# Optimization experiments

Hardware: AMD Instinct MI355X
Metric: run time of the kernel (lower is better)

Reference implementation:

```python
import jax, jax.numpy as jnp
import numpy as np

N = 4096
FIN = 256
FOUT = 256
H = 1  # num_heads MUST be 1: edge projections reshape [N,N,H] -> (1,N,N)
NEG_MASK = -1000000.0
LRELU_SLOPE = 0.2
ESP = 1e-06
LN_EPS = 1e-05


def setup_inputs() -> dict:
    key = jax.random.key(0)
    ks = jax.random.split(key, 9)
    nodes_features = jax.random.normal(ks[0], (N, FIN), dtype=jnp.float32)
    degree_matrix = jax.random.normal(ks[1], (N, N), dtype=jnp.float32)
    edges_features_distance = jax.random.uniform(ks[2], (N, N), dtype=jnp.float32)
    edges_features_bond = jax.random.uniform(ks[3], (N, N), dtype=jnp.float32)
    # learned parameters (xavier-ish scale)
    proj_param = jax.random.normal(ks[4], (H, FIN, FOUT), dtype=jnp.float32) * (1.0 / np.sqrt(FIN))
    a_src = jax.random.normal(ks[5], (H, FOUT, 1), dtype=jnp.float32) * (1.0 / np.sqrt(FOUT))
    a_tgt = jax.random.normal(ks[6], (H, FOUT, 1), dtype=jnp.float32) * (1.0 / np.sqrt(FOUT))
    w_dist = jax.random.normal(ks[7], (H, 1), dtype=jnp.float32)  # nn.Linear(1, H).weight
    w_bond = jax.random.normal(ks[8], (H, 1), dtype=jnp.float32)
    return {
        "nodes_features": nodes_features,
        "degree_matrix": degree_matrix,
        "edges_features_distance": edges_features_distance,
        "edges_features_bond": edges_features_bond,
        "proj_param": proj_param,
        "a_src": a_src,
        "a_tgt": a_tgt,
        "w_dist": w_dist,
        "w_bond": w_bond,
        "cutoff": 0,
    }


def reference(nodes_features, degree_matrix, edges_features_distance,
              edges_features_bond, proj_param, a_src, a_tgt, w_dist, w_bond,
              cutoff=0):
    n = nodes_features.shape[0]
    h, fin, fout = proj_param.shape
    # connectivity mask: keep degree where positive, else large negative
    connectivity_mask = jnp.where(degree_matrix > 0, degree_matrix, NEG_MASK)
    # node projection: [H, N, Fout] (dropout is identity in eval)
    proj = jnp.einsum('nf,hfo->hno', nodes_features, proj_param)
    # attention scores: outer-sum of per-node source/target scores
    s_src = jnp.einsum('hno,hoi->hni', proj, a_src)      # [H, N, 1]
    s_tgt = jnp.einsum('hno,hoi->hni', proj, a_tgt)      # [H, N, 1]
    all_scores = jax.nn.leaky_relu(s_src + jnp.swapaxes(s_tgt, 1, 2), LRELU_SLOPE)  # [H,N,N]
    # edge contributions: Linear(1, H) on scalar edge features, reshaped (1,N,N) (H==1)
    dist_c = ((-edges_features_distance)[..., None] * w_dist[:, 0]).reshape(1, n, n)
    bond_c = (edges_features_bond[..., None] * w_bond[:, 0]).reshape(1, n, n)
    all_scores = all_scores + dist_c + bond_c
    # masked softmax over neighbors
    attn = jax.nn.softmax(all_scores + connectivity_mask[None], axis=-1)  # [H,N,N]
    # weighted aggregation
    out = jnp.einsum('hnm,hmo->hno', attn, proj)  # [H, N, Fout]
    # faithful to torch: transpose(2,1) -> [H,Fout,N] then contiguous view(-1,H,Fout)
    out = jnp.transpose(out, (0, 2, 1)).reshape(-1, h, fout)
    # concat heads (skip connection and bias are disabled per init args)
    out = out.reshape(-1, h * fout)
    out = jax.nn.elu(out)  # ELU activation, alpha=1
    # ---- no_grad connectivity update ----
    o = jax.lax.stop_gradient(out)
    dm = jax.lax.stop_gradient(degree_matrix)
    sim = o @ o.T                                        # [N, N]
    decay = -jax.lax.stop_gradient(edges_features_distance)
    upd = jax.nn.sigmoid(sim) * decay * (dm > 0).astype(o.dtype)
    upd = upd + ESP
    mean = jnp.mean(upd, axis=-1, keepdims=True)
    var = jnp.mean(jnp.square(upd - mean), axis=-1, keepdims=True)
    upd = (upd - mean) / jnp.sqrt(var + LN_EPS)          # layer_norm, no affine
    upd = upd + upd.T
    return out, upd
```

## Files before the change

kernel.cpp:

```cpp
#include <hip/hip_runtime.h>


using f32x4  = __attribute__((ext_vector_type(4))) float;
using bf16x8 = __attribute__((ext_vector_type(8))) __bf16;
using bf16x4 = __attribute__((ext_vector_type(4))) __bf16;
using u32x4  = __attribute__((ext_vector_type(4))) unsigned int;

__global__ __launch_bounds__(256) void prep_kernel(const float* __restrict__ x,
                                                   __bf16* __restrict__ y,
                                                   const float* __restrict__ w,
                                                   __bf16* __restrict__ wt,
                                                   float* __restrict__ Lrow,
                                                   float* __restrict__ ssrc,
                                                   float* __restrict__ stgt) {
  const int bx = blockIdx.x;
  if (bx < 1024) {
    int i = (bx * 256 + threadIdx.x) * 4;
    f32x4 v = *(const f32x4*)(x + i);
    bf16x4 o = { (__bf16)v[0], (__bf16)v[1], (__bf16)v[2], (__bf16)v[3] };
    *(bf16x4*)(y + i) = o;
  } else {
    int wb = bx - 1024;
    int i = wb * 256 + threadIdx.x;
    int o = i >> 8, f = i & 255;
    wt[i] = (__bf16)w[f * 256 + o];
    if (wb < 16)              Lrow[wb * 256 + threadIdx.x] = 0.0f;
    else if (wb < 32)         ssrc[(wb - 16) * 256 + threadIdx.x] = 0.0f;
    else if (wb < 48)         stgt[(wb - 32) * 256 + threadIdx.x] = 0.0f;
  }
}

template<int BM, int BN, int MODE>
__global__ __launch_bounds__(256) void gemm_bf16_kernel(
    const __bf16* __restrict__ A, const __bf16* __restrict__ Bt,
    int M, int N, int K,
    float* __restrict__ outf, __bf16* __restrict__ outb,
    const float* __restrict__ e0, const float* __restrict__ e1,
    __bf16* __restrict__ axt, float* __restrict__ outt,
    float* __restrict__ bsum, float* __restrict__ bsq)
{
  constexpr int LDT = 72;
  constexpr int MI = BM / 32;
  constexpr int NI = BN / 32;
  __shared__ alignas(16) __bf16 As[BM * LDT];
  __shared__ alignas(16) __bf16 Bs[BN * LDT];
  const int tid  = threadIdx.x;
  const int lane = tid & 63;
  const int wid  = tid >> 6;
  const int wm0  = (wid >> 1) * (BM / 2);
  const int wn0  = (wid & 1) * (BN / 2);
  const int m0   = blockIdx.x * BM;
  const int n0   = blockIdx.y * BN;
  const int lr   = lane & 15;
  const int lk   = lane >> 4;

  f32x4 acc[MI][NI];
#pragma unroll
  for (int a = 0; a < MI; ++a)
#pragma unroll
    for (int b = 0; b < NI; ++b) acc[a][b] = (f32x4){0.f, 0.f, 0.f, 0.f};

  for (int kt = 0; kt < K; kt += 64) {
    __syncthreads();
    for (int idx = tid; idx < BM * 8; idx += 256) {
      int r = idx >> 3, c = idx & 7;
      u32x4 v = *(const u32x4*)(A + (size_t)(m0 + r) * K + kt + c * 8);
      *(u32x4*)(As + r * LDT + c * 8) = v;
    }
    for (int idx = tid; idx < BN * 8; idx += 256) {
      int r = idx >> 3, c = idx & 7;
      u32x4 v = *(const u32x4*)(Bt + (size_t)(n0 + r) * K + kt + c * 8);
      *(u32x4*)(Bs + r * LDT + c * 8) = v;
    }
    __syncthreads();
#pragma unroll
    for (int kk = 0; kk < 2; ++kk) {
      bf16x8 av[MI], bv[NI];
#pragma unroll
      for (int mi = 0; mi < MI; ++mi)
        av[mi] = *(const bf16x8*)(As + (wm0 + mi * 16 + lr) * LDT + kk * 32 + lk * 8);
#pragma unroll
      for (int ni = 0; ni < NI; ++ni)
        bv[ni] = *(const bf16x8*)(Bs + (wn0 + ni * 16 + lr) * LDT + kk * 32 + lk * 8);
#pragma unroll
      for (int mi = 0; mi < MI; ++mi)
#pragma unroll
        for (int ni = 0; ni < NI; ++ni)
          acc[mi][ni] = __builtin_amdgcn_mfma_f32_16x16x32_bf16(av[mi], bv[ni], acc[mi][ni], 0, 0, 0);
    }
  }

  if constexpr (MODE == 0) {
#pragma unroll
    for (int mi = 0; mi < MI; ++mi) {
#pragma unroll
      for (int j = 0; j < 4; ++j) {
        const int m = m0 + wm0 + mi * 16 + lk * 4 + j;
        float s1 = 0.f, s2 = 0.f;
#pragma unroll
        for (int ni = 0; ni < NI; ++ni) {
          const int n = n0 + wn0 + ni * 16 + lr;
          const float v = acc[mi][ni][j];
          outb[(size_t)n * 4096 + m] = (__bf16)v;
          s1 += v * e0[n];
          s2 += v * e1[n];
        }
#pragma unroll
        for (int o = 1; o < 16; o <<= 1) {
          s1 += __shfl_xor(s1, o, 64);
          s2 += __shfl_xor(s2, o, 64);
        }
        if (lr == 0) {
          atomicAdd(bsum + m, s1);
          atomicAdd(bsq + m, s2);
        }
      }
    }
  } else {
#pragma unroll
    for (int mi = 0; mi < MI; ++mi) {
#pragma unroll
      for (int j = 0; j < 4; ++j) {
        const int m = m0 + wm0 + mi * 16 + lk * 4 + j;
        float s = 0.f, s2 = 0.f;
#pragma unroll
        for (int ni = 0; ni < NI; ++ni) {
          const int n = n0 + wn0 + ni * 16 + lr;
          const size_t idx = (size_t)m * 4096 + n;
          const float v = acc[mi][ni][j];
          const float sg = 1.0f / (1.0f + __expf(-v));
          float tr;
          if constexpr (MODE == 2) {
            const float d = e0[idx];
            const float g = e1[idx];
            const float tval = sg * (-d) * (g > 0.f ? 1.0f : 0.0f) + 1e-6f;
            outt[idx] = tval;
            tr = tval;
          } else {
            const float a = (float)__builtin_nontemporal_load(axt + idx);
            const __bf16 tb = (__bf16)(sg * a + 1e-6f);
            axt[idx] = tb;
            tr = (float)tb;
          }
          s += tr;
          s2 += tr * tr;
        }
#pragma unroll
        for (int o = 1; o < 16; o <<= 1) {
          s  += __shfl_xor(s, o, 64);
          s2 += __shfl_xor(s2, o, 64);
        }
        if (lr == 0) {
          const int slot = blockIdx.y * 2 + (wid & 1);
          bsum[(size_t)slot * 4096 + m] = s;
          bsq [(size_t)slot * 4096 + m] = s2;
        }
      }
    }
  }
}

__global__ __launch_bounds__(256) void stats_small_kernel(
    const float* __restrict__ bsum, const float* __restrict__ bsq,
    float* __restrict__ mean, float* __restrict__ rstd)
{
  const int row = blockIdx.x * 256 + threadIdx.x;
  float S = 0.f, S2 = 0.f;
#pragma unroll 8
  for (int s = 0; s < 64; ++s) {
    S  += bsum[(size_t)s * 4096 + row];
    S2 += bsq [(size_t)s * 4096 + row];
  }
  const float m  = S * (1.0f / 4096.0f);
  const float var = S2 * (1.0f / 4096.0f) - m * m;
  mean[row] = m;
  rstd[row] = rsqrtf(var + 1e-5f);
}

__global__ __launch_bounds__(256) void score_exp_kernel(
    const float* __restrict__ dist, const float* __restrict__ bond,
    const float* __restrict__ deg,  const float* __restrict__ ssrc,
    const float* __restrict__ stgt, const float* __restrict__ wdp,
    const float* __restrict__ wbp,  __bf16* __restrict__ P,
    __bf16* __restrict__ aux,       float* __restrict__ Lrow)
{
  const float wd = wdp[0], wb = wbp[0];
  const int lane = threadIdx.x & 63;
  const size_t i = ((size_t)blockIdx.x * 256 + threadIdx.x) * 4;
  const int row = (int)(i >> 12);
  const int col = (int)(i & 4095);
  f32x4 d  = __builtin_nontemporal_load((const f32x4*)(dist + i));
  f32x4 g  = __builtin_nontemporal_load((const f32x4*)(deg + i));
  f32x4 b  = __builtin_nontemporal_load((const f32x4*)(bond + i));
  f32x4 st = *(const f32x4*)(stgt + col);
  const float si = ssrc[row];
  f32x4 p;
  bf16x4 pb, ab;
#pragma unroll
  for (int q = 0; q < 4; ++q) {
    float x = si + st[q];
    x = x > 0.f ? x : 0.2f * x;
    x += -d[q] * wd + b[q] * wb + (g[q] > 0.f ? g[q] : -1000000.0f);
    p[q] = __expf(x);
    pb[q] = (__bf16)p[q];
    ab[q] = (__bf16)(g[q] > 0.f ? -d[q] : 0.0f);
  }
  *(bf16x4*)(P + i) = pb;
  if (aux) *(bf16x4*)(aux + i) = ab;
  float s = p[0] + p[1] + p[2] + p[3];
#pragma unroll
  for (int o = 32; o; o >>= 1) s += __shfl_xor(s, o, 64);
  if (lane == 0) atomicAdd(Lrow + row, s);
}

__global__ __launch_bounds__(256) void gemm_splitk_kernel(
    const __bf16* __restrict__ A, const __bf16* __restrict__ Bt,
    __bf16* __restrict__ partial)
{
  constexpr int LDT = 72;
  __shared__ alignas(16) __bf16 As[64 * LDT];
  __shared__ alignas(16) __bf16 Bs[128 * LDT];
  const int tid  = threadIdx.x;
  const int lane = tid & 63;
  const int wid  = tid >> 6;
  const int wm0  = (wid >> 1) * 32;
  const int wn0  = (wid & 1) * 64;
  const int m0   = blockIdx.x * 64;
  const int n0   = blockIdx.y * 128;
  const int s    = blockIdx.z;
  const int lr   = lane & 15;
  const int lk   = lane >> 4;

  f32x4 acc[2][4];
#pragma unroll
  for (int a = 0; a < 2; ++a)
#pragma unroll
    for (int b = 0; b < 4; ++b) acc[a][b] = (f32x4){0.f, 0.f, 0.f, 0.f};

  const int k0 = s * 512;
  for (int kt = k0; kt < k0 + 512; kt += 64) {
    __syncthreads();
    for (int idx = tid; idx < 512; idx += 256) {
      int r = idx >> 3, c = idx & 7;
      u32x4 v = *(const u32x4*)(A + (size_t)(m0 + r) * 4096 + kt + c * 8);
      *(u32x4*)(As + r * LDT + c * 8) = v;
    }
    for (int idx = tid; idx < 1024; idx += 256) {
      int r = idx >> 3, c = idx & 7;
      u32x4 v = *(const u32x4*)(Bt + (size_t)(n0 + r) * 4096 + kt + c * 8);
      *(u32x4*)(Bs + r * LDT + c * 8) = v;
    }
    __syncthreads();
#pragma unroll
    for (int kk = 0; kk < 2; ++kk) {
      bf16x8 av[2], bv[4];
#pragma unroll
      for (int mi = 0; mi < 2; ++mi)
        av[mi] = *(const bf16x8*)(As + (wm0 + mi * 16 + lr) * LDT + kk * 32 + lk * 8);
#pragma unroll
      for (int ni = 0; ni < 4; ++ni)
        bv[ni] = *(const bf16x8*)(Bs + (wn0 + ni * 16 + lr) * LDT + kk * 32 + lk * 8);
#pragma unroll
      for (int mi = 0; mi < 2; ++mi)
#pragma unroll
        for (int ni = 0; ni < 4; ++ni)
          acc[mi][ni] = __builtin_amdgcn_mfma_f32_16x16x32_bf16(av[mi], bv[ni], acc[mi][ni], 0, 0, 0);
    }
  }

  __bf16* Pp = partial + (size_t)s * (4096 * 256);
#pragma unroll
  for (int mi = 0; mi < 2; ++mi)
#pragma unroll
    for (int ni = 0; ni < 4; ++ni)
#pragma unroll
      for (int j = 0; j < 4; ++j) {
        const int m = m0 + wm0 + mi * 16 + lk * 4 + j;
        const int n = n0 + wn0 + ni * 16 + lr;
        Pp[(size_t)m * 256 + n] = (__bf16)acc[mi][ni][j];
      }
}

__global__ __launch_bounds__(256) void reduce_elu_kernel(
    const __bf16* __restrict__ partial, const float* __restrict__ Lrow,
    float* __restrict__ out0, __bf16* __restrict__ E)
{
  __shared__ float tile[64][65];
  __shared__ float invL[64];
  const int tid = threadIdx.x;
  const int m0 = blockIdx.x * 64;
  const int f0 = blockIdx.y * 64;
  if (tid < 64) invL[tid] = 1.0f / Lrow[m0 + tid];
  f32x4 accv[4];
#pragma unroll
  for (int i = 0; i < 4; ++i) {
    int lin = i * 1024 + tid * 4;
    int r = lin >> 6, c = lin & 63;
    f32x4 sum = (f32x4){0.f, 0.f, 0.f, 0.f};
#pragma unroll
    for (int s = 0; s < 8; ++s) {
      bf16x4 pv = __builtin_nontemporal_load(
          (const bf16x4*)(partial + (size_t)s * (4096 * 256) +
                          (size_t)(m0 + r) * 256 + f0 + c));
#pragma unroll
      for (int q = 0; q < 4; ++q) sum[q] += (float)pv[q];
    }
    accv[i] = sum;
  }
  __syncthreads();
#pragma unroll
  for (int i = 0; i < 4; ++i) {
    int lin = i * 1024 + tid * 4;
    int r = lin >> 6, c = lin & 63;
    const float inv = invL[r];
    tile[r][c]     = accv[i][0] * inv;
    tile[r][c + 1] = accv[i][1] * inv;
    tile[r][c + 2] = accv[i][2] * inv;
    tile[r][c + 3] = accv[i][3] * inv;
  }
  __syncthreads();
#pragma unroll
  for (int i = 0; i < 4; ++i) {
    int lin = i * 1024 + tid * 4;
    int rr = lin >> 6, cc = lin & 63;
    f32x4 e;
#pragma unroll
    for (int q = 0; q < 4; ++q) {
      float v = tile[cc + q][rr];
      e[q] = v > 0.f ? v : expm1f(v);
    }
    size_t idx = (size_t)(f0 + rr) * 4096 + m0 + cc;
    __builtin_nontemporal_store(e, (f32x4*)(out0 + idx));
    bf16x4 eb = { (__bf16)e[0], (__bf16)e[1], (__bf16)e[2], (__bf16)e[3] };
    *(bf16x4*)(E + idx) = eb;
  }
}

__global__ __launch_bounds__(256) void finalize_bf16_kernel(
    const __bf16* __restrict__ tb, float* __restrict__ upd,
    const float* __restrict__ mean, const float* __restrict__ rstd)
{
  const int bj = blockIdx.x, bi = blockIdx.y;
  if (bi > bj) return;
  __shared__ float ta[64][65];
  __shared__ float tc[64][65];
  const int tid = threadIdx.x;
#pragma unroll
  for (int i = 0; i < 4; ++i) {
    int lin = i * 1024 + tid * 4;
    int r = lin >> 6, c = lin & 63;
    bf16x4 va = __builtin_nontemporal_load(
        (const bf16x4*)(tb + (size_t)(bi * 64 + r) * 4096 + bj * 64 + c));
    ta[r][c] = (float)va[0]; ta[r][c+1] = (float)va[1];
    ta[r][c+2] = (float)va[2]; ta[r][c+3] = (float)va[3];
  }
  if (bi != bj) {
#pragma unroll
    for (int i = 0; i < 4; ++i) {
      int lin = i * 1024 + tid * 4;
      int r = lin >> 6, c = lin & 63;
      bf16x4 vb = __builtin_nontemporal_load(
          (const bf16x4*)(tb + (size_t)(bj * 64 + r) * 4096 + bi * 64 + c));
      tc[r][c] = (float)vb[0]; tc[r][c+1] = (float)vb[1];
      tc[r][c+2] = (float)vb[2]; tc[r][c+3] = (float)vb[3];
    }
  }
  __syncthreads();
#pragma unroll
  for (int i = 0; i < 4; ++i) {
    int lin = i * 1024 + tid * 4;
    int r = lin >> 6, c = lin & 63;
    int gi = bi * 64 + r, gj = bj * 64 + c;
    const float mi_ = mean[gi], ri_ = rstd[gi];
    f32x4 mj = *(const f32x4*)(mean + gj);
    f32x4 rj = *(const f32x4*)(rstd + gj);
    f32x4 o;
#pragma unroll
    for (int q = 0; q < 4; ++q) {
      float v = (ta[r][c + q] - mi_) * ri_;
      float w = (bi == bj) ? (ta[c + q][r] - mj[q]) * rj[q]
                           : (tc[c + q][r] - mj[q]) * rj[q];
      o[q] = v + w;
    }
    __builtin_nontemporal_store(o, (f32x4*)(upd + (size_t)gi * 4096 + gj));
  }
  if (bi != bj) {
#pragma unroll
    for (int i = 0; i < 4; ++i) {
      int lin = i * 1024 + tid * 4;
      int r = lin >> 6, c = lin & 63;
      int gi = bj * 64 + r, gj = bi * 64 + c;
      const float mi_ = mean[gi], ri_ = rstd[gi];
      f32x4 mj = *(const f32x4*)(mean + gj);
      f32x4 rj = *(const f32x4*)(rstd + gj);
      f32x4 o;
#pragma unroll
      for (int q = 0; q < 4; ++q) {
        float v = (tc[r][c + q] - mi_) * ri_;
        float w = (ta[c + q][r] - mj[q]) * rj[q];
        o[q] = v + w;
      }
      __builtin_nontemporal_store(o, (f32x4*)(upd + (size_t)gi * 4096 + gj));
    }
  }
}

__global__ __launch_bounds__(256) void finalize_f32_kernel(
    float* __restrict__ t, const float* __restrict__ mean,
    const float* __restrict__ rstd)
{
  const int bj = blockIdx.x, bi = blockIdx.y;
  if (bi > bj) return;
  __shared__ float ta[64][65];
  __shared__ float tc[64][65];
  const int tid = threadIdx.x;
#pragma unroll
  for (int i = 0; i < 4; ++i) {
    int lin = i * 1024 + tid * 4;
    int r = lin >> 6, c = lin & 63;
    f32x4 va = *(const f32x4*)(t + (size_t)(bi * 64 + r) * 4096 + bj * 64 + c);
    ta[r][c] = va[0]; ta[r][c+1] = va[1]; ta[r][c+2] = va[2]; ta[r][c+3] = va[3];
  }
  if (bi != bj) {
#pragma unroll
    for (int i = 0; i < 4; ++i) {
      int lin = i * 1024 + tid * 4;
      int r = lin >> 6, c = lin & 63;
      f32x4 vb = *(const f32x4*)(t + (size_t)(bj * 64 + r) * 4096 + bi * 64 + c);
      tc[r][c] = vb[0]; tc[r][c+1] = vb[1]; tc[r][c+2] = vb[2]; tc[r][c+3] = vb[3];
    }
  }
  __syncthreads();
#pragma unroll
  for (int i = 0; i < 4; ++i) {
    int lin = i * 1024 + tid * 4;
    int r = lin >> 6, c = lin & 63;
    int gi = bi * 64 + r, gj = bj * 64 + c;
    const float mi_ = mean[gi], ri_ = rstd[gi];
    f32x4 mj = *(const f32x4*)(mean + gj);
    f32x4 rj = *(const f32x4*)(rstd + gj);
    f32x4 o;
#pragma unroll
    for (int q = 0; q < 4; ++q) {
      float v = (ta[r][c + q] - mi_) * ri_;
      float w = (bi == bj) ? (ta[c + q][r] - mj[q]) * rj[q]
                           : (tc[c + q][r] - mj[q]) * rj[q];
      o[q] = v + w;
    }
    *(f32x4*)(t + (size_t)gi * 4096 + gj) = o;
  }
  if (bi != bj) {
#pragma unroll
    for (int i = 0; i < 4; ++i) {
      int lin = i * 1024 + tid * 4;
      int r = lin >> 6, c = lin & 63;
      int gi = bj * 64 + r, gj = bi * 64 + c;
      const float mi_ = mean[gi], ri_ = rstd[gi];
      f32x4 mj = *(const f32x4*)(mean + gj);
      f32x4 rj = *(const f32x4*)(rstd + gj);
      f32x4 o;
#pragma unroll
      for (int q = 0; q < 4; ++q) {
        float v = (tc[r][c + q] - mi_) * ri_;
        float w = (ta[c + q][r] - mj[q]) * rj[q];
        o[q] = v + w;
      }
      *(f32x4*)(t + (size_t)gi * 4096 + gj) = o;
    }
  }
}

extern "C" void kernel_launch(void* const* d_in, const int* in_sizes, int n_in,
                              void* d_out, int out_size, void* d_ws, size_t ws_size,
                              hipStream_t stream) {
  const float* nodes  = (const float*)d_in[0];
  const float* degree = (const float*)d_in[1];
  const float* dist   = (const float*)d_in[2];
  const float* bond   = (const float*)d_in[3];
  const float* W      = (const float*)d_in[4];
  const float* a_src  = (const float*)d_in[5];
  const float* a_tgt  = (const float*)d_in[6];
  const float* w_dist = (const float*)d_in[7];
  const float* w_bond = (const float*)d_in[8];

  char* ws = (char*)d_ws;
  __bf16* nodesB = (__bf16*)ws;
  __bf16* Wt     = (__bf16*)(ws + (2u << 20));
  __bf16* projT  = (__bf16*)(ws + (2u << 20) + (256u << 10));
  __bf16* E      = (__bf16*)(ws + (9u << 20));
  float*  ssrc   = (float*)(ws + (11u << 20));
  float*  stgt   = ssrc + 4096;
  float*  mean   = stgt + 4096;
  float*  rstd   = mean + 4096;
  float*  Lrow   = rstd + 4096;

  const bool useAux = ws_size >= (size_t)(48u << 20);
  __bf16* aux  = useAux ? (__bf16*)(ws + (12u << 20)) : nullptr;
  float* Bsum  = useAux ? (float*)(ws + (44u << 20))
                        : (float*)(ws + (12u << 20));
  float* Bsq   = Bsum + (size_t)64 * 4096;

  float*  out0 = (float*)d_out;
  float*  t    = out0 + (size_t)4096 * 256;
  __bf16* P    = (__bf16*)t;
  __bf16* partials = (__bf16*)((char*)t + ((size_t)32 << 20));

  prep_kernel<<<1280, 256, 0, stream>>>(nodes, nodesB, W, Wt, Lrow, ssrc, stgt);

  gemm_bf16_kernel<64, 64, 0><<<dim3(64, 4), 256, 0, stream>>>(
      nodesB, Wt, 4096, 256, 256, nullptr, projT,
      a_src, a_tgt, nullptr, nullptr, ssrc, stgt);

  score_exp_kernel<<<16384, 256, 0, stream>>>(dist, bond, degree, ssrc, stgt,
                                              w_dist, w_bond, P, aux, Lrow);

  gemm_splitk_kernel<<<dim3(64, 2, 8), 256, 0, stream>>>(P, projT, partials);

  reduce_elu_kernel<<<dim3(64, 4), 256, 0, stream>>>(partials, Lrow, out0, E);

  if (useAux) {
    gemm_bf16_kernel<128, 128, 3><<<dim3(32, 32), 256, 0, stream>>>(
        E, E, 4096, 4096, 256, nullptr, nullptr,
        nullptr, nullptr, aux, nullptr, Bsum, Bsq);
    stats_small_kernel<<<16, 256, 0, stream>>>(Bsum, Bsq, mean, rstd);
    finalize_bf16_kernel<<<dim3(64, 64), 256, 0, stream>>>(aux, t, mean, rstd);
  } else {
    gemm_bf16_kernel<128, 128, 2><<<dim3(32, 32), 256, 0, stream>>>(
        E, E, 4096, 4096, 256, nullptr, nullptr,
        dist, degree, nullptr, t, Bsum, Bsq);
    stats_small_kernel<<<16, 256, 0, stream>>>(Bsum, Bsq, mean, rstd);
    finalize_f32_kernel<<<dim3(64, 64), 256, 0, stream>>>(t, mean, rstd);
  }
}
```

Baseline: 179.5 us.

## Fuse fp32-to-bf16 node conversion into projection GEMM and widen split-K blocks

Removes the separate pass that converted node features to bf16 by loading fp32 nodes directly in a new 512-thread projection GEMM and converting them while staging into shared memory. The split-K aggregation GEMM now uses 512-thread blocks covering all 256 output columns, which halves the grid and avoids loading each P tile twice. Both kernels prefetch global loads into registers before the barrier to overlap loads with the previous sync. The similarity GEMM is specialized into a fixed 128x128 kernel. Larger blocks reduce occupancy and grid size on the small GEMMs.

Measured after the change: 173.3 us. -3.4%, faster.

```diff
diff --git a/kernel.cpp b/kernel.cpp
--- a/kernel.cpp
+++ b/kernel.cpp
@@ -6,68 +6,150 @@
 using bf16x4 = __attribute__((ext_vector_type(4))) __bf16;
 using u32x4  = __attribute__((ext_vector_type(4))) unsigned int;
 
-__global__ __launch_bounds__(256) void prep_kernel(const float* __restrict__ x,
-                                                   __bf16* __restrict__ y,
-                                                   const float* __restrict__ w,
+__global__ __launch_bounds__(256) void prep_kernel(const float* __restrict__ w,
                                                    __bf16* __restrict__ wt,
                                                    float* __restrict__ Lrow,
                                                    float* __restrict__ ssrc,
                                                    float* __restrict__ stgt) {
   const int bx = blockIdx.x;
-  if (bx < 1024) {
-    int i = (bx * 256 + threadIdx.x) * 4;
-    f32x4 v = *(const f32x4*)(x + i);
-    bf16x4 o = { (__bf16)v[0], (__bf16)v[1], (__bf16)v[2], (__bf16)v[3] };
-    *(bf16x4*)(y + i) = o;
-  } else {
-    int wb = bx - 1024;
-    int i = wb * 256 + threadIdx.x;
-    int o = i >> 8, f = i & 255;
-    wt[i] = (__bf16)w[f * 256 + o];
-    if (wb < 16)              Lrow[wb * 256 + threadIdx.x] = 0.0f;
-    else if (wb < 32)         ssrc[(wb - 16) * 256 + threadIdx.x] = 0.0f;
-    else if (wb < 48)         stgt[(wb - 32) * 256 + threadIdx.x] = 0.0f;
-  }
-}
-
-template<int BM, int BN, int MODE>
-__global__ __launch_bounds__(256) void gemm_bf16_kernel(
-    const __bf16* __restrict__ A, const __bf16* __restrict__ Bt,
-    int M, int N, int K,
-    float* __restrict__ outf, __bf16* __restrict__ outb,
+  int i = bx * 256 + threadIdx.x;
+  int o = i >> 8, f = i & 255;
+  wt[i] = (__bf16)w[f * 256 + o];
+  if (bx < 16)       Lrow[bx * 256 + threadIdx.x] = 0.0f;
+  else if (bx < 32)  ssrc[(bx - 16) * 256 + threadIdx.x] = 0.0f;
+  else if (bx < 48)  stgt[(bx - 32) * 256 + threadIdx.x] = 0.0f;
+}
+
+__global__ __launch_bounds__(512) void proj_gemm_kernel(
+    const float* __restrict__ nodes, const __bf16* __restrict__ Wt,
+    __bf16* __restrict__ projT, const float* __restrict__ asrc,
+    const float* __restrict__ atgt, float* __restrict__ ssrc,
+    float* __restrict__ stgt)
+{
+  constexpr int LDT = 72;
+  __shared__ alignas(16) __bf16 As[64 * LDT];
+  __shared__ alignas(16) __bf16 Bs[128 * LDT];
+  const int tid  = threadIdx.x;
+  const int lane = tid & 63;
+  const int wid  = tid >> 6;
+  const int wm0  = (wid >> 2) * 32;
+  const int wn0  = (wid & 3) * 32;
+  const int m0   = blockIdx.x * 64;
+  const int n0   = blockIdx.y * 128;
+  const int lr   = lane & 15;
+  const int lk   = lane >> 4;
+  const int r    = tid >> 3;
+  const int c0   = (tid & 7) * 8;
+
+  f32x4 acc[2][2];
+#pragma unroll
+  for (int a = 0; a < 2; ++a)
+#pragma unroll
+    for (int b = 0; b < 2; ++b) acc[a][b] = (f32x4){0.f, 0.f, 0.f, 0.f};
+
+#pragma unroll
+  for (int it = 0; it < 4; ++it) {
+    const int kt = it * 64;
+    f32x4 a0 = __builtin_nontemporal_load(
+        (const f32x4*)(nodes + (size_t)(m0 + r) * 256 + kt + c0));
+    f32x4 a1 = __builtin_nontemporal_load(
+        (const f32x4*)(nodes + (size_t)(m0 + r) * 256 + kt + c0 + 4));
+    u32x4 bl[2];
+#pragma unroll
+    for (int i = 0; i < 2; ++i) {
+      int idx = i * 512 + tid;
+      int nB = idx >> 3, cB = idx & 7;
+      bl[i] = *(const u32x4*)(Wt + (size_t)(n0 + nB) * 256 + kt + cB * 8);
+    }
+    __syncthreads();
+    bf16x8 ab = { (__bf16)a0[0], (__bf16)a0[1], (__bf16)a0[2], (__bf16)a0[3],
+                  (__bf16)a1[0], (__bf16)a1[1], (__bf16)a1[2], (__bf16)a1[3] };
+    *(bf16x8*)(As + r * LDT + c0) = ab;
+#pragma unroll
+    for (int i = 0; i < 2; ++i) {
+      int idx = i * 512 + tid;
+      int nB = idx >> 3, cB = idx & 7;
+      *(u32x4*)(Bs + nB * LDT + cB * 8) = bl[i];
+    }
+    __syncthreads();
+#pragma unroll
+    for (int kk = 0; kk < 2; ++kk) {
+      bf16x8 av[2], bv[2];
+#pragma unroll
+      for (int mi = 0; mi < 2; ++mi)
+        av[mi] = *(const bf16x8*)(As + (wm0 + mi * 16 + lr) * LDT + kk * 32 + lk * 8);
+#pragma unroll
+      for (int ni = 0; ni < 2; ++ni)
+        bv[ni] = *(const bf16x8*)(Bs + (wn0 + ni * 16 + lr) * LDT + kk * 32 + lk * 8);
+#pragma unroll
+      for (int mi = 0; mi < 2; ++mi)
+#pragma unroll
+        for (int ni = 0; ni < 2; ++ni)
+          acc[mi][ni] = __builtin_amdgcn_mfma_f32_16x16x32_bf16(av[mi], bv[ni], acc[mi][ni], 0, 0, 0);
+    }
+  }
+
+#pragma unroll
+  for (int mi = 0; mi < 2; ++mi) {
+#pragma unroll
+    for (int j = 0; j < 4; ++j) {
+      const int m = m0 + wm0 + mi * 16 + lk * 4 + j;
+      float s1 = 0.f, s2 = 0.f;
+#pragma unroll
+      for (int ni = 0; ni < 2; ++ni) {
+        const int n = n0 + wn0 + ni * 16 + lr;
+        const float v = acc[mi][ni][j];
+        projT[(size_t)n * 4096 + m] = (__bf16)v;
+        s1 += v * asrc[n];
+        s2 += v * atgt[n];
+      }
+#pragma unroll
+      for (int o = 1; o < 16; o <<= 1) {
+        s1 += __shfl_xor(s1, o, 64);
+        s2 += __shfl_xor(s2, o, 64);
+      }
+      if (lr == 0) {
+        atomicAdd(ssrc + m, s1);
+        atomicAdd(stgt + m, s2);
+      }
+    }
+  }
+}
+
+template<int MODE>
+__global__ __launch_bounds__(256) void sim_gemm_kernel(
+    const __bf16* __restrict__ A, const __bf16* __restrict__ Bt, int K,
     const float* __restrict__ e0, const float* __restrict__ e1,
     __bf16* __restrict__ axt, float* __restrict__ outt,
     float* __restrict__ bsum, float* __restrict__ bsq)
 {
   constexpr int LDT = 72;
-  constexpr int MI = BM / 32;
-  constexpr int NI = BN / 32;
-  __shared__ alignas(16) __bf16 As[BM * LDT];
-  __shared__ alignas(16) __bf16 Bs[BN * LDT];
+  __shared__ alignas(16) __bf16 As[128 * LDT];
+  __shared__ alignas(16) __bf16 Bs[128 * LDT];
   const int tid  = threadIdx.x;
   const int lane = tid & 63;
   const int wid  = tid >> 6;
-  const int wm0  = (wid >> 1) * (BM / 2);
-  const int wn0  = (wid & 1) * (BN / 2);
-  const int m0   = blockIdx.x * BM;
-  const int n0   = blockIdx.y * BN;
+  const int wm0  = (wid >> 1) * 64;
+  const int wn0  = (wid & 1) * 64;
+  const int m0   = blockIdx.x * 128;
+  const int n0   = blockIdx.y * 128;
   const int lr   = lane & 15;
   const int lk   = lane >> 4;
 
-  f32x4 acc[MI][NI];
-#pragma unroll
-  for (int a = 0; a < MI; ++a)
-#pragma unroll
-    for (int b = 0; b < NI; ++b) acc[a][b] = (f32x4){0.f, 0.f, 0.f, 0.f};
+  f32x4 acc[4][4];
+#pragma unroll
+  for (int a = 0; a < 4; ++a)
+#pragma unroll
+    for (int b = 0; b < 4; ++b) acc[a][b] = (f32x4){0.f, 0.f, 0.f, 0.f};
 
   for (int kt = 0; kt < K; kt += 64) {
     __syncthreads();
-    for (int idx = tid; idx < BM * 8; idx += 256) {
+    for (int idx = tid; idx < 1024; idx += 256) {
       int r = idx >> 3, c = idx & 7;
       u32x4 v = *(const u32x4*)(A + (size_t)(m0 + r) * K + kt + c * 8);
       *(u32x4*)(As + r * LDT + c * 8) = v;
     }
-    for (int idx = tid; idx < BN * 8; idx += 256) {
+    for (int idx = tid; idx < 1024; idx += 256) {
       int r = idx >> 3, c = idx & 7;
       u32x4 v = *(const u32x4*)(Bt + (size_t)(n0 + r) * K + kt + c * 8);
       *(u32x4*)(Bs + r * LDT + c * 8) = v;
@@ -75,86 +157,58 @@
     __syncthreads();
 #pragma unroll
     for (int kk = 0; kk < 2; ++kk) {
-      bf16x8 av[MI], bv[NI];
-#pragma unroll
-      for (int mi = 0; mi < MI; ++mi)
+      bf16x8 av[4], bv[4];
+#pragma unroll
+      for (int mi = 0; mi < 4; ++mi)
         av[mi] = *(const bf16x8*)(As + (wm0 + mi * 16 + lr) * LDT + kk * 32 + lk * 8);
 #pragma unroll
-      for (int ni = 0; ni < NI; ++ni)
+      for (int ni = 0; ni < 4; ++ni)
         bv[ni] = *(const bf16x8*)(Bs + (wn0 + ni * 16 + lr) * LDT + kk * 32 + lk * 8);
 #pragma unroll
-      for (int mi = 0; mi < MI; ++mi)
-#pragma unroll
-        for (int ni = 0; ni < NI; ++ni)
+      for (int mi = 0; mi < 4; ++mi)
+#pragma unroll
+        for (int ni = 0; ni < 4; ++ni)
           acc[mi][ni] = __builtin_amdgcn_mfma_f32_16x16x32_bf16(av[mi], bv[ni], acc[mi][ni], 0, 0, 0);
     }
   }
 
-  if constexpr (MODE == 0) {
-#pragma unroll
-    for (int mi = 0; mi < MI; ++mi) {
-#pragma unroll
-      for (int j = 0; j < 4; ++j) {
-        const int m = m0 + wm0 + mi * 16 + lk * 4 + j;
-        float s1 = 0.f, s2 = 0.f;
-#pragma unroll
-        for (int ni = 0; ni < NI; ++ni) {
-          const int n = n0 + wn0 + ni * 16 + lr;
-          const float v = acc[mi][ni][j];
-          outb[(size_t)n * 4096 + m] = (__bf16)v;
-          s1 += v * e0[n];
-          s2 += v * e1[n];
+#pragma unroll
+  for (int mi = 0; mi < 4; ++mi) {
+#pragma unroll
+    for (int j = 0; j < 4; ++j) {
+      const int m = m0 + wm0 + mi * 16 + lk * 4 + j;
+      float s = 0.f, s2 = 0.f;
+#pragma unroll
+      for (int ni = 0; ni < 4; ++ni) {
+        const int n = n0 + wn0 + ni * 16 + lr;
+        const size_t idx = (size_t)m * 4096 + n;
+        const float v = acc[mi][ni][j];
+        const float sg = 1.0f / (1.0f + __expf(-v));
+        float tr;
+        if constexpr (MODE == 2) {
+          const float d = e0[idx];
+          const float g = e1[idx];
+          const float tval = sg * (-d) * (g > 0.f ? 1.0f : 0.0f) + 1e-6f;
+          outt[idx] = tval;
+          tr = tval;
+        } else {
+          const float a = (float)__builtin_nontemporal_load(axt + idx);
+          const __bf16 tb = (__bf16)(sg * a + 1e-6f);
+          axt[idx] = tb;
+          tr = (float)tb;
         }
-#pragma unroll
-        for (int o = 1; o < 16; o <<= 1) {
-          s1 += __shfl_xor(s1, o, 64);
-          s2 += __shfl_xor(s2, o, 64);
-        }
-        if (lr == 0) {
-          atomicAdd(bsum + m, s1);
-          atomicAdd(bsq + m, s2);
-        }
-      }
-    }
-  } else {
-#pragma unroll
-    for (int mi = 0; mi < MI; ++mi) {
-#pragma unroll
-      for (int j = 0; j < 4; ++j) {
-        const int m = m0 + wm0 + mi * 16 + lk * 4 + j;
-        float s = 0.f, s2 = 0.f;
-#pragma unroll
-        for (int ni = 0; ni < NI; ++ni) {
-          const int n = n0 + wn0 + ni * 16 + lr;
-          const size_t idx = (size_t)m * 4096 + n;
-          const float v = acc[mi][ni][j];
-          const float sg = 1.0f / (1.0f + __expf(-v));
-          float tr;
-          if constexpr (MODE == 2) {
-            const float d = e0[idx];
-            const float g = e1[idx];
-            const float tval = sg * (-d) * (g > 0.f ? 1.0f : 0.0f) + 1e-6f;
-            outt[idx] = tval;
-            tr = tval;
-          } else {
-            const float a = (float)__builtin_nontemporal_load(axt + idx);
-            const __bf16 tb = (__bf16)(sg * a + 1e-6f);
-            axt[idx] = tb;
-            tr = (float)tb;
-          }
-          s += tr;
-          s2 += tr * tr;
-        }
-#pragma unroll
-        for (int o = 1; o < 16; o <<= 1) {
-          s  += __shfl_xor(s, o, 64);
-          s2 += __shfl_xor(s2, o, 64);
-        }
-        if (lr == 0) {
-          const int slot = blockIdx.y * 2 + (wid & 1);
-          bsum[(size_t)slot * 4096 + m] = s;
-          bsq [(size_t)slot * 4096 + m] = s2;
-        }
+        s += tr;
+        s2 += tr * tr;
+      }
+#pragma unroll
+      for (int o = 1; o < 16; o <<= 1) {
+        s  += __shfl_xor(s, o, 64);
+        s2 += __shfl_xor(s2, o, 64);
+      }
+      if (lr == 0) {
+        const int slot = blockIdx.y * 2 + (wid & 1);
+        bsum[(size_t)slot * 4096 + m] = s;
+        bsq [(size_t)slot * 4096 + m] = s2;
       }
     }
   }
@@ -213,23 +267,23 @@
   if (lane == 0) atomicAdd(Lrow + row, s);
 }
 
-__global__ __launch_bounds__(256) void gemm_splitk_kernel(
+__global__ __launch_bounds__(512) void gemm_splitk_kernel(
     const __bf16* __restrict__ A, const __bf16* __restrict__ Bt,
     __bf16* __restrict__ partial)
 {
   constexpr int LDT = 72;
   __shared__ alignas(16) __bf16 As[64 * LDT];
-  __shared__ alignas(16) __bf16 Bs[128 * LDT];
+  __shared__ alignas(16) __bf16 Bs[256 * LDT];
   const int tid  = threadIdx.x;
   const int lane = tid & 63;
   const int wid  = tid >> 6;
-  const int wm0  = (wid >> 1) * 32;
-  const int wn0  = (wid & 1) * 64;
+  const int wm0  = (wid >> 2) * 32;
+  const int wn0  = (wid & 3) * 64;
   const int m0   = blockIdx.x * 64;
-  const int n0   = blockIdx.y * 128;
-  const int s    = blockIdx.z;
+  const int s    = blockIdx.y;
   const int lr   = lane & 15;
   const int lk   = lane >> 4;
+  const int rA   = tid >> 3, cA = tid & 7;
 
   f32x4 acc[2][4];
 #pragma unroll
@@ -239,16 +293,21 @@
 
   const int k0 = s * 512;
   for (int kt = k0; kt < k0 + 512; kt += 64) {
+    u32x4 va = *(const u32x4*)(A + (size_t)(m0 + rA) * 4096 + kt + cA * 8);
+    u32x4 vb[4];
+#pragma unroll
+    for (int i = 0; i < 4; ++i) {
+      int idx = i * 512 + tid;
+      int rB = idx >> 3, cB = idx & 7;
+      vb[i] = *(const u32x4*)(Bt + (size_t)rB * 4096 + kt + cB * 8);
+    }
     __syncthreads();
-    for (int idx = tid; idx < 512; idx += 256) {
-      int r = idx >> 3, c = idx & 7;
-      u32x4 v = *(const u32x4*)(A + (size_t)(m0 + r) * 4096 + kt + c * 8);
-      *(u32x4*)(As + r * LDT + c * 8) = v;
-    }
-    for (int idx = tid; idx < 1024; idx += 256) {
-      int r = idx >> 3, c = idx & 7;
-      u32x4 v = *(const u32x4*)(Bt + (size_t)(n0 + r) * 4096 + kt + c * 8);
-      *(u32x4*)(Bs + r * LDT + c * 8) = v;
+    *(u32x4*)(As + rA * LDT + cA * 8) = va;
+#pragma unroll
+    for (int i = 0; i < 4; ++i) {
+      int idx = i * 512 + tid;
+      int rB = idx >> 3, cB = idx & 7;
+      *(u32x4*)(Bs + rB * LDT + cB * 8) = vb[i];
     }
     __syncthreads();
 #pragma unroll
@@ -276,7 +335,7 @@
 #pragma unroll
       for (int j = 0; j < 4; ++j) {
         const int m = m0 + wm0 + mi * 16 + lk * 4 + j;
-        const int n = n0 + wn0 + ni * 16 + lr;
+        const int n = wn0 + ni * 16 + lr;
         Pp[(size_t)m * 256 + n] = (__bf16)acc[mi][ni][j];
       }
 }
@@ -484,7 +543,6 @@
   const float* w_bond = (const float*)d_in[8];
 
   char* ws = (char*)d_ws;
-  __bf16* nodesB = (__bf16*)ws;
   __bf16* Wt     = (__bf16*)(ws + (2u << 20));
   __bf16* projT  = (__bf16*)(ws + (2u << 20) + (256u << 10));
   __bf16* E      = (__bf16*)(ws + (9u << 20));
@@ -505,29 +563,26 @@
   __bf16* P    = (__bf16*)t;
   __bf16* partials = (__bf16*)((char*)t + ((size_t)32 << 20));
 
-  prep_kernel<<<1280, 256, 0, stream>>>(nodes, nodesB, W, Wt, Lrow, ssrc, stgt);
-
-  gemm_bf16_kernel<64, 64, 0><<<dim3(64, 4), 256, 0, stream>>>(
-      nodesB, Wt, 4096, 256, 256, nullptr, projT,
-      a_src, a_tgt, nullptr, nullptr, ssrc, stgt);
+  prep_kernel<<<256, 256, 0, stream>>>(W, Wt, Lrow, ssrc, stgt);
+
+  proj_gemm_kernel<<<dim3(64, 2), 512, 0, stream>>>(
+      nodes, Wt, projT, a_src, a_tgt, ssrc, stgt);
 
   score_exp_kernel<<<16384, 256, 0, stream>>>(dist, bond, degree, ssrc, stgt,
                                               w_dist, w_bond, P, aux, Lrow);
 
-  gemm_splitk_kernel<<<dim3(64, 2, 8), 256, 0, stream>>>(P, projT, partials);
+  gemm_splitk_kernel<<<dim3(64, 8), 512, 0, stream>>>(P, projT, partials);
 
   reduce_elu_kernel<<<dim3(64, 4), 256, 0, stream>>>(partials, Lrow, out0, E);
 
   if (useAux) {
-    gemm_bf16_kernel<128, 128, 3><<<dim3(32, 32), 256, 0, stream>>>(
-        E, E, 4096, 4096, 256, nullptr, nullptr,
-        nullptr, nullptr, aux, nullptr, Bsum, Bsq);
+    sim_gemm_kernel<3><<<dim3(32, 32), 256, 0, stream>>>(
+        E, E, 256, nullptr, nullptr, aux, nullptr, Bsum, Bsq);
     stats_small_kernel<<<16, 256, 0, stream>>>(Bsum, Bsq, mean, rstd);
     finalize_bf16_kernel<<<dim3(64, 64), 256, 0, stream>>>(aux, t, mean, rstd);
   } else {
-    gemm_bf16_kernel<128, 128, 2><<<dim3(32, 32), 256, 0, stream>>>(
-        E, E, 4096, 4096, 256, nullptr, nullptr,
-        dist, degree, nullptr, t, Bsum, Bsq);
+    sim_gemm_kernel<2><<<dim3(32, 32), 256, 0, stream>>>(
+        E, E, 256, dist, degree, nullptr, t, Bsum, Bsq);
     stats_small_kernel<<<16, 256, 0, stream>>>(Bsum, Bsq, mean, rstd);
     finalize_f32_kernel<<<dim3(64, 64), 256, 0, stream>>>(t, mean, rstd);
   }
```
